# Optimization experiments

Hardware: AMD Instinct MI355X
Metric: run time of the kernel (lower is better)

The kernel has to match this reference:

```python
import jax, jax.numpy as jnp
import numpy as np

N = 4194304  # number of sampled points (flattened)
W = 32       # hidden width
IN_PTS, IN_VIEWS = 3, 3


def setup_inputs() -> dict:
    key = jax.random.key(0)
    ks = jax.random.split(key, 13)
    def lin(k, fan_in, fan_out):
        # torch nn.Linear default init: U(-1/sqrt(fan_in), 1/sqrt(fan_in))
        bound = 1.0 / np.sqrt(fan_in)
        kw, kb = jax.random.split(k)
        w = jax.random.uniform(kw, (fan_in, fan_out), jnp.float32, -bound, bound)
        b = jax.random.uniform(kb, (fan_out,), jnp.float32, -bound, bound)
        return w, b
    x = jax.random.normal(ks[0], (N, IN_PTS + IN_VIEWS), jnp.float32)
    w0, b0 = lin(ks[1], IN_PTS, W)          # pts_linears[0]
    w1, b1 = lin(ks[2], W, W)               # pts_linears[1]
    wf, bf = lin(ks[3], W, W)               # feature_linear
    ws, bs = lin(ks[4], W, 1)               # sigma_linear
    wv, bv = lin(ks[5], IN_VIEWS + W, W)    # view_linears[0]
    wr, br = lin(ks[6], W, 3)               # rgb_linear
    return {"x": x, "w0": w0, "b0": b0, "w1": w1, "b1": b1,
            "wf": wf, "bf": bf, "ws": ws, "bs": bs,
            "wv": wv, "bv": bv, "wr": wr, "br": br}


def reference(x, w0, b0, w1, b1, wf, bf, ws, bs, wv, bv, wr, br):
    pts, views = x[..., :IN_PTS], x[..., IN_PTS:]
    h = jax.nn.relu(pts @ w0 + b0)
    h = jax.nn.relu(h @ w1 + b1)
    sigma = h @ ws + bs                     # [N, 1]
    feature = h @ wf + bf                   # [N, W]
    h = jnp.concatenate([feature, views], axis=-1)  # [N, W+3]
    h = jax.nn.relu(h @ wv + bv)
    rgb = h @ wr + br                       # [N, 3]
    return jnp.concatenate([rgb, sigma], axis=-1)   # [N, 4]
```

## Files before the change

### kernel.cpp

```cpp
#include <hip/hip_runtime.h>


#define NPTS   4194304
#define NT32   (NPTS / 32)

typedef _Float16 f16;
typedef _Float16 f16x2 __attribute__((ext_vector_type(2)));
typedef _Float16 f16x8 __attribute__((ext_vector_type(8)));
typedef __fp16   h16x2 __attribute__((ext_vector_type(2)));
typedef float    f32x16 __attribute__((ext_vector_type(16)));

union H8 { f16x8 v; unsigned u[4]; };

static __device__ __forceinline__ unsigned pkrtz(float a, float b) {
    return __builtin_bit_cast(unsigned, __builtin_amdgcn_cvt_pkrtz(a, b));
}
static __device__ __forceinline__ unsigned relu2(unsigned w) {
    f16x2 h = __builtin_bit_cast(f16x2, w);
    f16x2 z = (f16x2)(f16)0.f;
    return __builtin_bit_cast(unsigned, __builtin_elementwise_max(h, z));
}
static __device__ __forceinline__ float fdot2(unsigned a, unsigned b, float c) {
    return __builtin_amdgcn_fdot2(__builtin_bit_cast(h16x2, a),
                                  __builtin_bit_cast(h16x2, b), c, false);
}

#define MFMA32(A, B, C) __builtin_amdgcn_mfma_f32_32x32x16_f16((A), (B), (C), 0, 0, 0)

__global__ __launch_bounds__(1024) void kilonerf_prep(
    const float* __restrict__ wf, const float* __restrict__ bf,
    const float* __restrict__ wv, const float* __restrict__ bv,
    float* __restrict__ ws_out)
{
    const int tid = threadIdx.x;
    const int k = tid >> 5, m = tid & 31;
    float acc = 0.f;
#pragma unroll 8
    for (int t = 0; t < 32; ++t)
        acc = fmaf(wf[k * 32 + t], wv[t * 32 + m], acc);
    ws_out[k * 32 + m] = acc;
    if (tid < 32) {
        float b = bv[tid];
#pragma unroll 8
        for (int t = 0; t < 32; ++t)
            b = fmaf(bf[t], wv[t * 32 + tid], b);
        ws_out[1024 + tid] = b;
    }
}

__global__ __launch_bounds__(256, 4) void kilonerf_r15(
    const float* __restrict__ x,
    const float* __restrict__ w0, const float* __restrict__ b0,
    const float* __restrict__ w1, const float* __restrict__ b1,
    const float* __restrict__ ws, const float* __restrict__ bs,
    const float* __restrict__ wv, const float* __restrict__ wr,
    const float* __restrict__ br,
    const float* __restrict__ wsp,
    float* __restrict__ out)
{
    const int lane = threadIdx.x & 63;
    const int m  = lane & 31;
    const int hi = lane >> 5;

    int sj[8], row[16];
#pragma unroll
    for (int j = 0; j < 8; ++j)  sj[j]  = (j & 3) + 8 * (j >> 2) + 4 * hi;
#pragma unroll
    for (int r = 0; r < 16; ++r) row[r] = (r & 3) + 8 * (r >> 2) + 4 * hi;

    const float* Wc    = wsp;
    const float* bvEff = wsp + 1024;

    f16x8 aw0x, awv2x, aw1lo, aw1hi, awclo, awchi, awrlo, awrhi;
#pragma unroll
    for (int j = 0; j < 8; ++j) {
        const int k = sj[j];
        aw0x[j]  = (k < 3) ? (f16)w0[k * 32 + m]
                  : (k == 3 ? (f16)b0[m] : (f16)0.f);
        awv2x[j] = (k >= 4 && k < 7) ? (f16)wv[(32 + (k - 4)) * 32 + m]
                  : (k == 7 ? (f16)bvEff[m] : (f16)0.f);
        aw1lo[j] = (f16)w1[k * 32 + m];
        aw1hi[j] = (f16)w1[(16 + k) * 32 + m];
        awclo[j] = (f16)Wc[k * 32 + m];
        awchi[j] = (f16)Wc[(16 + k) * 32 + m];
        awrlo[j] = (m < 3) ? (f16)wr[k * 3 + m] : (f16)0.f;
        awrhi[j] = (m < 3) ? (f16)wr[(16 + k) * 3 + m] : (f16)0.f;
    }

    unsigned wspk[8];
#pragma unroll
    for (int w = 0; w < 8; ++w)
        wspk[w] = pkrtz(ws[row[2 * w]], ws[row[2 * w + 1]]);

    f32x16 b1c;
#pragma unroll
    for (int r = 0; r < 16; ++r) b1c[r] = b1[row[r]];

    const float br0 = br[0], br1 = br[1], br2 = br[2], bs0 = bs[0];

    f32x16 zf;
#pragma unroll
    for (int r = 0; r < 16; ++r) zf[r] = 0.f;

    const int wslot  = blockIdx.x * 4 + (threadIdx.x >> 6);
    const int nslots = gridDim.x * 4;

    float2 cx0, cx1, cx2;
    {
        const float2* xp2 = reinterpret_cast<const float2*>(
            x + (size_t)(wslot * 32 + m) * 6);
        cx0 = xp2[0]; cx1 = xp2[1]; cx2 = xp2[2];
    }

    for (int tile = wslot; tile < NT32; tile += nslots) {
        int np = tile + nslots; if (np >= NT32) np = wslot;
        const float2* xn = reinterpret_cast<const float2*>(
            x + (size_t)(np * 32 + m) * 6);
        float2 nx0 = xn[0], nx1 = xn[1], nx2 = xn[2];

        const float fa = hi ? cx1.y : cx0.x;
        const float fb = hi ? cx2.x : cx0.y;
        const float fc = hi ? cx2.y : cx1.x;
        H8 bx;
        bx.u[0] = pkrtz(fa, fb);
        bx.u[1] = pkrtz(fc, 1.0f);
        bx.u[2] = 0u;
        bx.u[3] = 0u;

        f32x16 c0 = MFMA32(aw0x, bx.v, zf);

        H8 blo, bhi;
        blo.u[0] = relu2(pkrtz(c0[0], c0[1]));
        blo.u[1] = relu2(pkrtz(c0[2], c0[3]));
        blo.u[2] = relu2(pkrtz(c0[4], c0[5]));
        blo.u[3] = relu2(pkrtz(c0[6], c0[7]));
        bhi.u[0] = relu2(pkrtz(c0[8], c0[9]));
        bhi.u[1] = relu2(pkrtz(c0[10], c0[11]));
        bhi.u[2] = relu2(pkrtz(c0[12], c0[13]));
        bhi.u[3] = relu2(pkrtz(c0[14], c0[15]));

        f32x16 c1 = MFMA32(aw1lo, blo.v, b1c);
        c1 = MFMA32(aw1hi, bhi.v, c1);

        blo.u[0] = relu2(pkrtz(c1[0], c1[1]));
        blo.u[1] = relu2(pkrtz(c1[2], c1[3]));
        blo.u[2] = relu2(pkrtz(c1[4], c1[5]));
        blo.u[3] = relu2(pkrtz(c1[6], c1[7]));
        bhi.u[0] = relu2(pkrtz(c1[8], c1[9]));
        bhi.u[1] = relu2(pkrtz(c1[10], c1[11]));
        bhi.u[2] = relu2(pkrtz(c1[12], c1[13]));
        bhi.u[3] = relu2(pkrtz(c1[14], c1[15]));

        float s0 = 0.f, s1 = 0.f;
#pragma unroll
        for (int w = 0; w < 4; ++w) {
            s0 = fdot2(blo.u[w], wspk[w], s0);
            s1 = fdot2(bhi.u[w], wspk[4 + w], s1);
        }
        float sg = s0 + s1;
        sg += __shfl_xor(sg, 32);

        f32x16 cv = MFMA32(awv2x, bx.v, zf);

        cv = MFMA32(awclo, blo.v, cv);
        cv = MFMA32(awchi, bhi.v, cv);

        blo.u[0] = relu2(pkrtz(cv[0], cv[1]));
        blo.u[1] = relu2(pkrtz(cv[2], cv[3]));
        blo.u[2] = relu2(pkrtz(cv[4], cv[5]));
        blo.u[3] = relu2(pkrtz(cv[6], cv[7]));
        bhi.u[0] = relu2(pkrtz(cv[8], cv[9]));
        bhi.u[1] = relu2(pkrtz(cv[10], cv[11]));
        bhi.u[2] = relu2(pkrtz(cv[12], cv[13]));
        bhi.u[3] = relu2(pkrtz(cv[14], cv[15]));

        f32x16 cr = MFMA32(awrlo, blo.v, zf);
        cr = MFMA32(awrhi, bhi.v, cr);

        if (hi == 0) {
            float4 o = make_float4(cr[0] + br0, cr[1] + br1,
                                   cr[2] + br2, sg + bs0);
            *reinterpret_cast<float4*>(out + (size_t)(tile * 32 + m) * 4) = o;
        }

        cx0 = nx0; cx1 = nx1; cx2 = nx2;
    }
}

extern "C" void kernel_launch(void* const* d_in, const int* in_sizes, int n_in,
                              void* d_out, int out_size, void* d_ws, size_t ws_size,
                              hipStream_t stream) {
    const float* x  = (const float*)d_in[0];
    const float* w0 = (const float*)d_in[1];
    const float* b0 = (const float*)d_in[2];
    const float* w1 = (const float*)d_in[3];
    const float* b1 = (const float*)d_in[4];
    const float* wf = (const float*)d_in[5];
    const float* bf = (const float*)d_in[6];
    const float* ws = (const float*)d_in[7];
    const float* bs = (const float*)d_in[8];
    const float* wv = (const float*)d_in[9];
    const float* bv = (const float*)d_in[10];
    const float* wr = (const float*)d_in[11];
    const float* br = (const float*)d_in[12];
    float* out = (float*)d_out;
    float* wsp = (float*)d_ws;

    kilonerf_prep<<<dim3(1), dim3(1024), 0, stream>>>(wf, bf, wv, bv, wsp);

    dim3 block(256);
    dim3 grid(2048);
    kilonerf_r15<<<grid, block, 0, stream>>>(x, w0, b0, w1, b1,
                                             ws, bs, wv, wr, br, wsp, out);
}
```

Measured before the change: 57.47 us.

## Process two 32-point tiles per wave iteration and split MFMA accumulation chains

```diff
diff --git a/kernel.cpp b/kernel.cpp
--- a/kernel.cpp
+++ b/kernel.cpp
@@ -48,7 +48,7 @@
     }
 }
 
-__global__ __launch_bounds__(256, 4) void kilonerf_r15(
+__global__ __launch_bounds__(256, 2) void kilonerf_r17(
     const float* __restrict__ x,
     const float* __restrict__ w0, const float* __restrict__ b0,
     const float* __restrict__ w1, const float* __restrict__ b1,
@@ -104,86 +104,143 @@
 
     const int wslot  = blockIdx.x * 4 + (threadIdx.x >> 6);
     const int nslots = gridDim.x * 4;
-
-    float2 cx0, cx1, cx2;
+    const int npairs = NT32 / 2;
+
+    float2 ax0, ax1, ax2, bx0, bx1, bx2;
     {
-        const float2* xp2 = reinterpret_cast<const float2*>(
-            x + (size_t)(wslot * 32 + m) * 6);
-        cx0 = xp2[0]; cx1 = xp2[1]; cx2 = xp2[2];
-    }
-
-    for (int tile = wslot; tile < NT32; tile += nslots) {
-        int np = tile + nslots; if (np >= NT32) np = wslot;
-        const float2* xn = reinterpret_cast<const float2*>(
-            x + (size_t)(np * 32 + m) * 6);
-        float2 nx0 = xn[0], nx1 = xn[1], nx2 = xn[2];
-
-        const float fa = hi ? cx1.y : cx0.x;
-        const float fb = hi ? cx2.x : cx0.y;
-        const float fc = hi ? cx2.y : cx1.x;
-        H8 bx;
-        bx.u[0] = pkrtz(fa, fb);
-        bx.u[1] = pkrtz(fc, 1.0f);
-        bx.u[2] = 0u;
-        bx.u[3] = 0u;
-
-        f32x16 c0 = MFMA32(aw0x, bx.v, zf);
-
-        H8 blo, bhi;
-        blo.u[0] = relu2(pkrtz(c0[0], c0[1]));
-        blo.u[1] = relu2(pkrtz(c0[2], c0[3]));
-        blo.u[2] = relu2(pkrtz(c0[4], c0[5]));
-        blo.u[3] = relu2(pkrtz(c0[6], c0[7]));
-        bhi.u[0] = relu2(pkrtz(c0[8], c0[9]));
-        bhi.u[1] = relu2(pkrtz(c0[10], c0[11]));
-        bhi.u[2] = relu2(pkrtz(c0[12], c0[13]));
-        bhi.u[3] = relu2(pkrtz(c0[14], c0[15]));
-
-        f32x16 c1 = MFMA32(aw1lo, blo.v, b1c);
-        c1 = MFMA32(aw1hi, bhi.v, c1);
-
-        blo.u[0] = relu2(pkrtz(c1[0], c1[1]));
-        blo.u[1] = relu2(pkrtz(c1[2], c1[3]));
-        blo.u[2] = relu2(pkrtz(c1[4], c1[5]));
-        blo.u[3] = relu2(pkrtz(c1[6], c1[7]));
-        bhi.u[0] = relu2(pkrtz(c1[8], c1[9]));
-        bhi.u[1] = relu2(pkrtz(c1[10], c1[11]));
-        bhi.u[2] = relu2(pkrtz(c1[12], c1[13]));
-        bhi.u[3] = relu2(pkrtz(c1[14], c1[15]));
-
-        float s0 = 0.f, s1 = 0.f;
+        const float2* pa = reinterpret_cast<const float2*>(
+            x + (size_t)(wslot * 64 + m) * 6);
+        const float2* pb = reinterpret_cast<const float2*>(
+            x + (size_t)(wslot * 64 + 32 + m) * 6);
+        ax0 = pa[0]; ax1 = pa[1]; ax2 = pa[2];
+        bx0 = pb[0]; bx1 = pb[1]; bx2 = pb[2];
+    }
+
+    for (int pair = wslot; pair < npairs; pair += nslots) {
+        int np = pair + nslots; if (np >= npairs) np = wslot;
+        const float2* pa = reinterpret_cast<const float2*>(
+            x + (size_t)(np * 64 + m) * 6);
+        const float2* pb = reinterpret_cast<const float2*>(
+            x + (size_t)(np * 64 + 32 + m) * 6);
+        float2 nax0 = pa[0], nax1 = pa[1], nax2 = pa[2];
+        float2 nbx0 = pb[0], nbx1 = pb[1], nbx2 = pb[2];
+
+        H8 bxA, bxB;
+        {
+            const float fa = hi ? ax1.y : ax0.x;
+            const float fb = hi ? ax2.x : ax0.y;
+            const float fc = hi ? ax2.y : ax1.x;
+            bxA.u[0] = pkrtz(fa, fb); bxA.u[1] = pkrtz(fc, 1.0f);
+            bxA.u[2] = 0u; bxA.u[3] = 0u;
+        }
+        {
+            const float fa = hi ? bx1.y : bx0.x;
+            const float fb = hi ? bx2.x : bx0.y;
+            const float fc = hi ? bx2.y : bx1.x;
+            bxB.u[0] = pkrtz(fa, fb); bxB.u[1] = pkrtz(fc, 1.0f);
+            bxB.u[2] = 0u; bxB.u[3] = 0u;
+        }
+
+        f32x16 c0A = MFMA32(aw0x,  bxA.v, zf);
+        f32x16 c0B = MFMA32(aw0x,  bxB.v, zf);
+        f32x16 cvA = MFMA32(awv2x, bxA.v, zf);
+        f32x16 cvB = MFMA32(awv2x, bxB.v, zf);
+
+        H8 loA, hiA, loB, hiB;
+        loA.u[0] = relu2(pkrtz(c0A[0], c0A[1]));
+        loA.u[1] = relu2(pkrtz(c0A[2], c0A[3]));
+        loA.u[2] = relu2(pkrtz(c0A[4], c0A[5]));
+        loA.u[3] = relu2(pkrtz(c0A[6], c0A[7]));
+        hiA.u[0] = relu2(pkrtz(c0A[8], c0A[9]));
+        hiA.u[1] = relu2(pkrtz(c0A[10], c0A[11]));
+        hiA.u[2] = relu2(pkrtz(c0A[12], c0A[13]));
+        hiA.u[3] = relu2(pkrtz(c0A[14], c0A[15]));
+        loB.u[0] = relu2(pkrtz(c0B[0], c0B[1]));
+        loB.u[1] = relu2(pkrtz(c0B[2], c0B[3]));
+        loB.u[2] = relu2(pkrtz(c0B[4], c0B[5]));
+        loB.u[3] = relu2(pkrtz(c0B[6], c0B[7]));
+        hiB.u[0] = relu2(pkrtz(c0B[8], c0B[9]));
+        hiB.u[1] = relu2(pkrtz(c0B[10], c0B[11]));
+        hiB.u[2] = relu2(pkrtz(c0B[12], c0B[13]));
+        hiB.u[3] = relu2(pkrtz(c0B[14], c0B[15]));
+
+        f32x16 p0A = MFMA32(aw1lo, loA.v, b1c);
+        f32x16 p1A = MFMA32(aw1hi, hiA.v, zf);
+        f32x16 p0B = MFMA32(aw1lo, loB.v, b1c);
+        f32x16 p1B = MFMA32(aw1hi, hiB.v, zf);
+        f32x16 c1A = p0A + p1A;
+        f32x16 c1B = p0B + p1B;
+
+        loA.u[0] = relu2(pkrtz(c1A[0], c1A[1]));
+        loA.u[1] = relu2(pkrtz(c1A[2], c1A[3]));
+        loA.u[2] = relu2(pkrtz(c1A[4], c1A[5]));
+        loA.u[3] = relu2(pkrtz(c1A[6], c1A[7]));
+        hiA.u[0] = relu2(pkrtz(c1A[8], c1A[9]));
+        hiA.u[1] = relu2(pkrtz(c1A[10], c1A[11]));
+        hiA.u[2] = relu2(pkrtz(c1A[12], c1A[13]));
+        hiA.u[3] = relu2(pkrtz(c1A[14], c1A[15]));
+        loB.u[0] = relu2(pkrtz(c1B[0], c1B[1]));
+        loB.u[1] = relu2(pkrtz(c1B[2], c1B[3]));
+        loB.u[2] = relu2(pkrtz(c1B[4], c1B[5]));
+        loB.u[3] = relu2(pkrtz(c1B[6], c1B[7]));
+        hiB.u[0] = relu2(pkrtz(c1B[8], c1B[9]));
+        hiB.u[1] = relu2(pkrtz(c1B[10], c1B[11]));
+        hiB.u[2] = relu2(pkrtz(c1B[12], c1B[13]));
+        hiB.u[3] = relu2(pkrtz(c1B[14], c1B[15]));
+
+        float sA0 = 0.f, sA1 = 0.f, sB0 = 0.f, sB1 = 0.f;
 #pragma unroll
         for (int w = 0; w < 4; ++w) {
-            s0 = fdot2(blo.u[w], wspk[w], s0);
-            s1 = fdot2(bhi.u[w], wspk[4 + w], s1);
-        }
-        float sg = s0 + s1;
-        sg += __shfl_xor(sg, 32);
-
-        f32x16 cv = MFMA32(awv2x, bx.v, zf);
-
-        cv = MFMA32(awclo, blo.v, cv);
-        cv = MFMA32(awchi, bhi.v, cv);
-
-        blo.u[0] = relu2(pkrtz(cv[0], cv[1]));
-        blo.u[1] = relu2(pkrtz(cv[2], cv[3]));
-        blo.u[2] = relu2(pkrtz(cv[4], cv[5]));
-        blo.u[3] = relu2(pkrtz(cv[6], cv[7]));
-        bhi.u[0] = relu2(pkrtz(cv[8], cv[9]));
-        bhi.u[1] = relu2(pkrtz(cv[10], cv[11]));
-        bhi.u[2] = relu2(pkrtz(cv[12], cv[13]));
-        bhi.u[3] = relu2(pkrtz(cv[14], cv[15]));
-
-        f32x16 cr = MFMA32(awrlo, blo.v, zf);
-        cr = MFMA32(awrhi, bhi.v, cr);
+            sA0 = fdot2(loA.u[w], wspk[w], sA0);
+            sA1 = fdot2(hiA.u[w], wspk[4 + w], sA1);
+            sB0 = fdot2(loB.u[w], wspk[w], sB0);
+            sB1 = fdot2(hiB.u[w], wspk[4 + w], sB1);
+        }
+        float sgA = sA0 + sA1; sgA += __shfl_xor(sgA, 32);
+        float sgB = sB0 + sB1; sgB += __shfl_xor(sgB, 32);
+
+        f32x16 q0A = MFMA32(awclo, loA.v, cvA);
+        f32x16 q1A = MFMA32(awchi, hiA.v, zf);
+        f32x16 q0B = MFMA32(awclo, loB.v, cvB);
+        f32x16 q1B = MFMA32(awchi, hiB.v, zf);
+        f32x16 ccA = q0A + q1A;
+        f32x16 ccB = q0B + q1B;
+
+        loA.u[0] = relu2(pkrtz(ccA[0], ccA[1]));
+        loA.u[1] = relu2(pkrtz(ccA[2], ccA[3]));
+        loA.u[2] = relu2(pkrtz(ccA[4], ccA[5]));
+        loA.u[3] = relu2(pkrtz(ccA[6], ccA[7]));
+        hiA.u[0] = relu2(pkrtz(ccA[8], ccA[9]));
+        hiA.u[1] = relu2(pkrtz(ccA[10], ccA[11]));
+        hiA.u[2] = relu2(pkrtz(ccA[12], ccA[13]));
+        hiA.u[3] = relu2(pkrtz(ccA[14], ccA[15]));
+        loB.u[0] = relu2(pkrtz(ccB[0], ccB[1]));
+        loB.u[1] = relu2(pkrtz(ccB[2], ccB[3]));
+        loB.u[2] = relu2(pkrtz(ccB[4], ccB[5]));
+        loB.u[3] = relu2(pkrtz(ccB[6], ccB[7]));
+        hiB.u[0] = relu2(pkrtz(ccB[8], ccB[9]));
+        hiB.u[1] = relu2(pkrtz(ccB[10], ccB[11]));
+        hiB.u[2] = relu2(pkrtz(ccB[12], ccB[13]));
+        hiB.u[3] = relu2(pkrtz(ccB[14], ccB[15]));
+
+        f32x16 r0A = MFMA32(awrlo, loA.v, zf);
+        f32x16 r1A = MFMA32(awrhi, hiA.v, zf);
+        f32x16 r0B = MFMA32(awrlo, loB.v, zf);
+        f32x16 r1B = MFMA32(awrhi, hiB.v, zf);
 
         if (hi == 0) {
-            float4 o = make_float4(cr[0] + br0, cr[1] + br1,
-                                   cr[2] + br2, sg + bs0);
-            *reinterpret_cast<float4*>(out + (size_t)(tile * 32 + m) * 4) = o;
-        }
-
-        cx0 = nx0; cx1 = nx1; cx2 = nx2;
+            float4 oA = make_float4(r0A[0] + r1A[0] + br0,
+                                    r0A[1] + r1A[1] + br1,
+                                    r0A[2] + r1A[2] + br2, sgA + bs0);
+            float4 oB = make_float4(r0B[0] + r1B[0] + br0,
+                                    r0B[1] + r1B[1] + br1,
+                                    r0B[2] + r1B[2] + br2, sgB + bs0);
+            *reinterpret_cast<float4*>(out + (size_t)(pair * 64 + m) * 4) = oA;
+            *reinterpret_cast<float4*>(out + (size_t)(pair * 64 + 32 + m) * 4) = oB;
+        }
+
+        ax0 = nax0; ax1 = nax1; ax2 = nax2;
+        bx0 = nbx0; bx1 = nbx1; bx2 = nbx2;
     }
 }
 
@@ -210,6 +267,6 @@
 
     dim3 block(256);
     dim3 grid(2048);
-    kilonerf_r15<<<grid, block, 0, stream>>>(x, w0, b0, w1, b1,
+    kilonerf_r17<<<grid, block, 0, stream>>>(x, w0, b0, w1, b1,
                                              ws, bs, wv, wr, br, wsp, out);
 }
```

Result: slower. 61.14 us (+6.4%).
